# Performance work log

Measured on AMD Instinct MI355X. Metric: run time of the kernel, lower is better.

## Reference

```python
import jax, jax.numpy as jnp
import numpy as np

B, H, W, C = 32, 512, 512, 3
NUM_MASKS = 2
MASK_H, MASK_W = 128, 128


def setup_inputs() -> dict:
    key = jax.random.key(0)
    k1, k2, k3 = jax.random.split(key, 3)
    inputs = jax.random.uniform(k1, (B, H, W, C), dtype=jnp.float32) * 255.0
    centers_y = jax.random.randint(k2, (B, NUM_MASKS), 0, H, dtype=jnp.int32)
    centers_x = jax.random.randint(k3, (B, NUM_MASKS), 0, W, dtype=jnp.int32)
    return {"inputs": inputs, "centers_y": centers_y, "centers_x": centers_x}


def reference(inputs, centers_y, centers_x):
    # Same math as the TF layer: for each image and each mask, zero the
    # rectangle [cy - mh//2, cy + mh//2) x [cx - mw//2, cx + mw//2), clipped
    # to image bounds. Vectorized over batch and masks via coordinate compares.
    h = inputs.shape[1]
    w = inputs.shape[2]
    y1 = jnp.clip(centers_y - MASK_H // 2, 0, h)  # [B, M]
    y2 = jnp.clip(centers_y + MASK_H // 2, 0, h)
    x1 = jnp.clip(centers_x - MASK_W // 2, 0, w)
    x2 = jnp.clip(centers_x + MASK_W // 2, 0, w)
    rows = jnp.arange(h, dtype=jnp.int32)  # [H]
    cols = jnp.arange(w, dtype=jnp.int32)  # [W]
    in_y = (rows[None, None, :] >= y1[:, :, None]) & (rows[None, None, :] < y2[:, :, None])  # [B,M,H]
    in_x = (cols[None, None, :] >= x1[:, :, None]) & (cols[None, None, :] < x2[:, :, None])  # [B,M,W]
    cut = jnp.any(in_y[:, :, :, None] & in_x[:, :, None, :], axis=1)  # [B,H,W]
    keep = jnp.logical_not(cut)[..., None].astype(inputs.dtype)  # [B,H,W,1]
    return inputs * keep
```

## Files before the change

### kernel.cpp

```cpp
#include <hip/hip_runtime.h>
#include <climits>


#define BB 32
#define HH 512
#define WW 512
#define ROW4 384
#define HALF 64

__global__ __launch_bounds__(128)
void RandomCutout_59545426592097_kernel(const float4* __restrict__ in,
                                        const int* __restrict__ cys,
                                        const int* __restrict__ cxs,
                                        float4* __restrict__ out) {
    const int row  = blockIdx.x;
    const int b    = row >> 9;
    const int y    = row & (HH - 1);
    const int base = row * ROW4;
    const int t    = threadIdx.x;

    const float4* __restrict__ src = in + base;
    float4* __restrict__ dst       = out + base;

    float4 v0 = src[t];
    float4 v1 = src[t + 128];
    float4 v2 = src[t + 256];

    const int cy0 = cys[2 * b + 0];
    const int cy1 = cys[2 * b + 1];
    const bool yin_a = (y >= cy0 - HALF) & (y < cy0 + HALF);
    const bool yin_b = (y >= cy1 - HALF) & (y < cy1 + HALF);

    if (yin_a | yin_b) {
        const int cx0 = cxs[2 * b + 0];
        const int cx1 = cxs[2 * b + 1];
        const int A1 = 3 * (cx0 - HALF);
        const int A2 = yin_a ? 3 * (cx0 + HALF) : INT_MIN;
        const int B1 = 3 * (cx1 - HALF);
        const int B2 = yin_b ? 3 * (cx1 + HALF) : INT_MIN;

        const int p0 = t * 4;
        const int p1 = (t + 128) * 4;
        const int p2 = (t + 256) * 4;

#define CUT(p) ((((p) >= A1) & ((p) < A2)) | (((p) >= B1) & ((p) < B2)))
        if (CUT(p0 + 0)) v0.x = 0.0f;
        if (CUT(p0 + 1)) v0.y = 0.0f;
        if (CUT(p0 + 2)) v0.z = 0.0f;
        if (CUT(p0 + 3)) v0.w = 0.0f;

        if (CUT(p1 + 0)) v1.x = 0.0f;
        if (CUT(p1 + 1)) v1.y = 0.0f;
        if (CUT(p1 + 2)) v1.z = 0.0f;
        if (CUT(p1 + 3)) v1.w = 0.0f;

        if (CUT(p2 + 0)) v2.x = 0.0f;
        if (CUT(p2 + 1)) v2.y = 0.0f;
        if (CUT(p2 + 2)) v2.z = 0.0f;
        if (CUT(p2 + 3)) v2.w = 0.0f;
#undef CUT
    }

    dst[t]       = v0;
    dst[t + 128] = v1;
    dst[t + 256] = v2;
}

extern "C" void kernel_launch(void* const* d_in, const int* in_sizes, int n_in,
                              void* d_out, int out_size, void* d_ws, size_t ws_size,
                              hipStream_t stream) {
    const float4* in  = (const float4*)d_in[0];
    const int*    cys = (const int*)d_in[1];
    const int*    cxs = (const int*)d_in[2];
    float4*       out = (float4*)d_out;

    const int threads = 128;
    const int blocks  = BB * HH;
    RandomCutout_59545426592097_kernel<<<blocks, threads, 0, stream>>>(in, cys, cxs, out);
}
```

Baseline: 177.3 us.

## Process eight rows per block with hoisted column masks and nontemporal stores

Each block now handles eight consecutive image rows using 384 threads, with one float4 column per thread. The per-lane column cut masks are computed once and reused across all eight rows, and each row only does its row test. Outputs are written with nontemporal stores to avoid polluting cache. The block count drops 8x and each thread keeps eight loads in flight, which raises register use per thread.

```diff
diff --git a/kernel.cpp b/kernel.cpp
--- a/kernel.cpp
+++ b/kernel.cpp
@@ -1,80 +1,74 @@
 #include <hip/hip_runtime.h>
-#include <climits>
 
 
 #define BB 32
 #define HH 512
-#define WW 512
 #define ROW4 384
 #define HALF 64
+#define RPB 8
+#define TPB 384
 
-__global__ __launch_bounds__(128)
-void RandomCutout_59545426592097_kernel(const float4* __restrict__ in,
+typedef float f32x4 __attribute__((ext_vector_type(4)));
+
+__global__ __launch_bounds__(TPB)
+void RandomCutout_59545426592097_kernel(const f32x4* __restrict__ in,
                                         const int* __restrict__ cys,
                                         const int* __restrict__ cxs,
-                                        float4* __restrict__ out) {
-    const int row  = blockIdx.x;
-    const int b    = row >> 9;
-    const int y    = row & (HH - 1);
-    const int base = row * ROW4;
-    const int t    = threadIdx.x;
+                                        f32x4* __restrict__ out) {
+    const int blk = blockIdx.x;
+    const int b   = blk >> 6;
+    const int y0  = (blk & 63) << 3;
+    const int t   = threadIdx.x;
 
-    const float4* __restrict__ src = in + base;
-    float4* __restrict__ dst       = out + base;
+    const int base = (b * HH + y0) * ROW4;
+    const f32x4* __restrict__ src = in + base;
+    f32x4* __restrict__ dst       = out + base;
 
-    float4 v0 = src[t];
-    float4 v1 = src[t + 128];
-    float4 v2 = src[t + 256];
+    f32x4 v[RPB];
+#pragma unroll
+    for (int r = 0; r < RPB; ++r) v[r] = src[r * ROW4 + t];
 
     const int cy0 = cys[2 * b + 0];
     const int cy1 = cys[2 * b + 1];
-    const bool yin_a = (y >= cy0 - HALF) & (y < cy0 + HALF);
-    const bool yin_b = (y >= cy1 - HALF) & (y < cy1 + HALF);
+    const int cx0 = cxs[2 * b + 0];
+    const int cx1 = cxs[2 * b + 1];
 
-    if (yin_a | yin_b) {
-        const int cx0 = cxs[2 * b + 0];
-        const int cx1 = cxs[2 * b + 1];
-        const int A1 = 3 * (cx0 - HALF);
-        const int A2 = yin_a ? 3 * (cx0 + HALF) : INT_MIN;
-        const int B1 = 3 * (cx1 - HALF);
-        const int B2 = yin_b ? 3 * (cx1 + HALF) : INT_MIN;
+    const int A1 = 3 * (cx0 - HALF), A2 = 3 * (cx0 + HALF);
+    const int B1 = 3 * (cx1 - HALF), B2 = 3 * (cx1 + HALF);
 
-        const int p0 = t * 4;
-        const int p1 = (t + 128) * 4;
-        const int p2 = (t + 256) * 4;
+    const int p = t * 4;
+    const bool a0 = (p + 0 >= A1) & (p + 0 < A2);
+    const bool a1 = (p + 1 >= A1) & (p + 1 < A2);
+    const bool a2 = (p + 2 >= A1) & (p + 2 < A2);
+    const bool a3 = (p + 3 >= A1) & (p + 3 < A2);
+    const bool b0 = (p + 0 >= B1) & (p + 0 < B2);
+    const bool b1 = (p + 1 >= B1) & (p + 1 < B2);
+    const bool b2 = (p + 2 >= B1) & (p + 2 < B2);
+    const bool b3 = (p + 3 >= B1) & (p + 3 < B2);
 
-#define CUT(p) ((((p) >= A1) & ((p) < A2)) | (((p) >= B1) & ((p) < B2)))
-        if (CUT(p0 + 0)) v0.x = 0.0f;
-        if (CUT(p0 + 1)) v0.y = 0.0f;
-        if (CUT(p0 + 2)) v0.z = 0.0f;
-        if (CUT(p0 + 3)) v0.w = 0.0f;
-
-        if (CUT(p1 + 0)) v1.x = 0.0f;
-        if (CUT(p1 + 1)) v1.y = 0.0f;
-        if (CUT(p1 + 2)) v1.z = 0.0f;
-        if (CUT(p1 + 3)) v1.w = 0.0f;
-
-        if (CUT(p2 + 0)) v2.x = 0.0f;
-        if (CUT(p2 + 1)) v2.y = 0.0f;
-        if (CUT(p2 + 2)) v2.z = 0.0f;
-        if (CUT(p2 + 3)) v2.w = 0.0f;
-#undef CUT
+#pragma unroll
+    for (int r = 0; r < RPB; ++r) {
+        const int y = y0 + r;
+        const bool ya = (y >= cy0 - HALF) & (y < cy0 + HALF);
+        const bool yb = (y >= cy1 - HALF) & (y < cy1 + HALF);
+        if (ya | yb) {
+            if ((ya & a0) | (yb & b0)) v[r].x = 0.0f;
+            if ((ya & a1) | (yb & b1)) v[r].y = 0.0f;
+            if ((ya & a2) | (yb & b2)) v[r].z = 0.0f;
+            if ((ya & a3) | (yb & b3)) v[r].w = 0.0f;
+        }
+        __builtin_nontemporal_store(v[r], &dst[r * ROW4 + t]);
     }
-
-    dst[t]       = v0;
-    dst[t + 128] = v1;
-    dst[t + 256] = v2;
 }
 
 extern "C" void kernel_launch(void* const* d_in, const int* in_sizes, int n_in,
                               void* d_out, int out_size, void* d_ws, size_t ws_size,
                               hipStream_t stream) {
-    const float4* in  = (const float4*)d_in[0];
-    const int*    cys = (const int*)d_in[1];
-    const int*    cxs = (const int*)d_in[2];
-    float4*       out = (float4*)d_out;
+    const f32x4* in  = (const f32x4*)d_in[0];
+    const int*   cys = (const int*)d_in[1];
+    const int*   cxs = (const int*)d_in[2];
+    f32x4*       out = (f32x4*)d_out;
 
-    const int threads = 128;
-    const int blocks  = BB * HH;
-    RandomCutout_59545426592097_kernel<<<blocks, threads, 0, stream>>>(in, cys, cxs, out);
+    const int blocks = BB * (HH / RPB);
+    RandomCutout_59545426592097_kernel<<<blocks, TPB, 0, stream>>>(in, cys, cxs, out);
 }
```

New measurement: 179.8 us. No clear change (+1.4%).
